# Performance work log

Measured on AMD Instinct MI355X. Metric: run time of the kernel, lower is better.

## Reference

```python
import jax, jax.numpy as jnp
import numpy as np

N = 50000
E = 800000
G = 2500  # number of graphs


def setup_inputs() -> dict:
    key = jax.random.key(0)
    ks = jax.random.split(key, 10)
    x = jax.random.normal(ks[0], (N, 128), dtype=jnp.float32)
    edge_index = jax.random.randint(ks[1], (2, E), 0, N, dtype=jnp.int64)
    batch = jnp.sort(jax.random.randint(ks[2], (N,), 0, G, dtype=jnp.int64))
    def lin(k, fan_in, shape):
        return jax.random.normal(k, shape, dtype=jnp.float32) / np.sqrt(fan_in)
    return {
        'x': x, 'edge_index': edge_index, 'batch': batch,
        'W1': lin(ks[3], 128, (128, 64)), 'b1': jnp.zeros((64,), jnp.float32),
        'W2': lin(ks[4], 64, (64, 64)),  'b2': jnp.zeros((64,), jnp.float32),
        'W3': lin(ks[5], 64, (64, 64)),  'b3': jnp.zeros((64,), jnp.float32),
        'Wp1': lin(ks[6], 64, (64, 64)), 'bp1': jnp.zeros((64,), jnp.float32),
        'Wp2': lin(ks[7], 64, (64, 32)), 'bp2': jnp.zeros((32,), jnp.float32),
    }


def _gcn_norm(edge_index, n_nodes):
    # PyG GCNConv default: add self-loops, symmetric normalization
    loops = jnp.arange(n_nodes, dtype=edge_index.dtype)
    src = jnp.concatenate([edge_index[0], loops])
    dst = jnp.concatenate([edge_index[1], loops])
    deg = jax.ops.segment_sum(jnp.ones_like(dst, dtype=jnp.float32), dst,
                              num_segments=n_nodes)
    dis = jnp.where(deg > 0, jax.lax.rsqrt(deg), 0.0)
    norm = dis[src] * dis[dst]  # [E + N]
    return src, dst, norm


def _gcn_conv(x, W, b, src, dst, norm, n_nodes):
    h = x @ W                                   # transform first (small dim)
    m = h[src] * norm[:, None]                  # gather + scale
    out = jax.ops.segment_sum(m, dst, num_segments=n_nodes)  # scatter-add
    return out + b


def reference(x, edge_index, batch, W1, b1, W2, b2, W3, b3, Wp1, bp1, Wp2, bp2):
    n_nodes = x.shape[0]
    src, dst, norm = _gcn_norm(edge_index, n_nodes)
    x1 = jax.nn.relu(_gcn_conv(x, W1, b1, src, dst, norm, n_nodes))
    x2 = jax.nn.relu(_gcn_conv(x1, W2, b2, src, dst, norm, n_nodes))
    x3 = jax.nn.relu(_gcn_conv(x2, W3, b3, src, dst, norm, n_nodes))
    h = x1 + x2 + x3
    # global_mean_pool
    sums = jax.ops.segment_sum(h, batch, num_segments=G)
    counts = jax.ops.segment_sum(jnp.ones((n_nodes,), jnp.float32), batch,
                                 num_segments=G)
    pooled = sums / jnp.maximum(counts, 1.0)[:, None]
    z = jax.nn.relu(pooled @ Wp1 + bp1) @ Wp2 + bp2
    return z
```

## Files before the change

kernel.cpp:

```cpp
#include <hip/hip_runtime.h>
#include <math.h>


typedef short short8 __attribute__((ext_vector_type(8)));
typedef float f32x4 __attribute__((ext_vector_type(4)));

__device__ inline float bf2f(unsigned short h) {
    return __uint_as_float((unsigned)h << 16);
}
__device__ inline unsigned short f2bf(float f) {
    unsigned u = __float_as_uint(f);
    return (unsigned short)((u + (0x7FFFu + ((u >> 16) & 1u))) >> 16);
}
__device__ inline void bh8f(short8 u, float4& a, float4& b) {
    a.x = bf2f((unsigned short)u[0]); a.y = bf2f((unsigned short)u[1]);
    a.z = bf2f((unsigned short)u[2]); a.w = bf2f((unsigned short)u[3]);
    b.x = bf2f((unsigned short)u[4]); b.y = bf2f((unsigned short)u[5]);
    b.z = bf2f((unsigned short)u[6]); b.w = bf2f((unsigned short)u[7]);
}
__device__ inline float4 f4fma(float s, float4 a, float4 acc) {
    acc.x += s * a.x; acc.y += s * a.y; acc.z += s * a.z; acc.w += s * a.w;
    return acc;
}

__global__ void kA_hist(const int* __restrict__ dst, int* __restrict__ hist,
                        int E, int chunk) {
    __shared__ int h[256];
    int t = threadIdx.x;
    h[t] = 0;
    __syncthreads();
    int e0 = blockIdx.x * chunk;
    int e1 = min(e0 + chunk, E);
    for (int e = e0 + t; e < e1; e += 256) atomicAdd(&h[dst[e] >> 8], 1);
    __syncthreads();
    hist[blockIdx.x * 256 + t] = h[t];
}

__global__ void kA_colscan(const int* __restrict__ hist, int* __restrict__ cursorA,
                           int* __restrict__ tot) {
    __shared__ int s[256];
    int t = threadIdx.x;
    int k = blockIdx.x;
    int v = hist[t * 256 + k];
    s[t] = v;
    __syncthreads();
    for (int st = 1; st < 256; st <<= 1) {
        int u = s[t];
        if (t >= st) u += s[t - st];
        __syncthreads();
        s[t] = u;
        __syncthreads();
    }
    cursorA[t * 256 + k] = s[t] - v;
    if (t == 255) tot[k] = s[255];
}

__global__ void kA_scatter(const int* __restrict__ src, const int* __restrict__ dst,
                           const int* __restrict__ cursorA, const int* __restrict__ tot,
                           unsigned* __restrict__ ebuf, int E, int chunk) {
    __shared__ int s[256];
    __shared__ int cur[256];
    int t = threadIdx.x;
    s[t] = tot[t];
    __syncthreads();
    for (int st = 1; st < 256; st <<= 1) {
        int u = s[t];
        if (t >= st) u += s[t - st];
        __syncthreads();
        s[t] = u;
        __syncthreads();
    }
    int bstart = (t == 0) ? 0 : s[t - 1];
    cur[t] = cursorA[blockIdx.x * 256 + t] + bstart;
    __syncthreads();
    int e0 = blockIdx.x * chunk;
    int e1 = min(e0 + chunk, E);
    for (int e = e0 + t; e < e1; e += 256) {
        int d = dst[e];
        int p = atomicAdd(&cur[d >> 8], 1);
        ebuf[p] = ((unsigned)(d & 255) << 24) | (unsigned)src[e];
    }
}

__global__ void kB1(const unsigned* __restrict__ ebuf, const int* __restrict__ tot,
                    float* __restrict__ dis, int* __restrict__ offs, int N, int E) {
    __shared__ int s[256];
    __shared__ int h[256];
    int t = threadIdx.x;
    int k = blockIdx.x;
    s[t] = tot[t];
    __syncthreads();
    for (int st = 1; st < 256; st <<= 1) {
        int u = s[t];
        if (t >= st) u += s[t - st];
        __syncthreads();
        s[t] = u;
        __syncthreads();
    }
    int lo = (k == 0) ? 0 : s[k - 1];
    int hi = s[k];
    h[t] = 0;
    __syncthreads();
    for (int p = lo + t; p < hi; p += 256) atomicAdd(&h[ebuf[p] >> 24], 1);
    __syncthreads();
    int c = h[t];
    int node = k * 256 + t;
    if (node < N) dis[node] = rsqrtf((float)(c + 1));
    s[t] = c;
    __syncthreads();
    for (int st = 1; st < 256; st <<= 1) {
        int u = s[t];
        if (t >= st) u += s[t - st];
        __syncthreads();
        s[t] = u;
        __syncthreads();
    }
    if (node < N) offs[node] = lo + s[t] - c;
    if (node == N - 1) offs[N] = E;
}

__global__ void kB2(const unsigned* __restrict__ ebuf, const int* __restrict__ tot,
                    const float* __restrict__ dis, const int* __restrict__ offs,
                    float2* __restrict__ col2, int N, int E) {
    __shared__ int s[256];
    __shared__ int cur[256];
    int t = threadIdx.x;
    int k = blockIdx.x;
    s[t] = tot[t];
    __syncthreads();
    for (int st = 1; st < 256; st <<= 1) {
        int u = s[t];
        if (t >= st) u += s[t - st];
        __syncthreads();
        s[t] = u;
        __syncthreads();
    }
    int lo = (k == 0) ? 0 : s[k - 1];
    int hi = s[k];
    int node = k * 256 + t;
    cur[t] = (node < N) ? offs[node] : 0;
    __syncthreads();
    for (int p = lo + t; p < hi; p += 256) {
        unsigned e = ebuf[p];
        int srcI = (int)(e & 0x00FFFFFFu);
        int q = atomicAdd(&cur[e >> 24], 1);
        col2[q] = make_float2(__int_as_float(srcI), dis[srcI]);
    }
}


template <int K>
__global__ __launch_bounds__(256) void k_gemm_f32(const float* __restrict__ X,
                                                  const float* __restrict__ W,
                                                  unsigned short* __restrict__ H, int n) {
    __shared__ short wt[64 * K];
    int t = threadIdx.x;
    for (int idx = t; idx < 64 * K; idx += 256) {
        int k = idx >> 6, ch = idx & 63;
        wt[ch * K + k] = (short)f2bf(W[idx]);
    }
    __syncthreads();
    int wave = t >> 6, lane = t & 63;
    int q = lane >> 4, l = lane & 15;
    int tile = blockIdx.x * 4 + wave;
    if (tile * 16 >= n) return;
    int node = tile * 16 + l;
    short8 afr[4][K / 32];
#pragma unroll
    for (int mb = 0; mb < 4; mb++)
#pragma unroll
        for (int s = 0; s < K / 32; s++)
            afr[mb][s] = *(const short8*)(wt + (mb * 16 + l) * K + s * 32 + q * 8);
    f32x4 acc[4] = {};
    const float* xr = X + (size_t)node * K + q * 8;
#pragma unroll
    for (int s = 0; s < K / 32; s++) {
        float4 xa = *(const float4*)(xr + s * 32);
        float4 xb = *(const float4*)(xr + s * 32 + 4);
        short8 bfr;
        bfr[0] = (short)f2bf(xa.x); bfr[1] = (short)f2bf(xa.y);
        bfr[2] = (short)f2bf(xa.z); bfr[3] = (short)f2bf(xa.w);
        bfr[4] = (short)f2bf(xb.x); bfr[5] = (short)f2bf(xb.y);
        bfr[6] = (short)f2bf(xb.z); bfr[7] = (short)f2bf(xb.w);
#pragma unroll
        for (int mb = 0; mb < 4; mb++)
            acc[mb] = __builtin_amdgcn_mfma_f32_16x16x32_bf16(afr[mb][s], bfr, acc[mb], 0, 0, 0);
    }
#pragma unroll
    for (int mb = 0; mb < 4; mb++) {
        ushort4 u;
        u.x = f2bf(acc[mb][0]); u.y = f2bf(acc[mb][1]);
        u.z = f2bf(acc[mb][2]); u.w = f2bf(acc[mb][3]);
        ushort4* slab = (ushort4*)H + (size_t)(mb >> 1) * (size_t)n * 8;
        slab[(size_t)node * 8 + (mb & 1) * 4 + q] = u;
    }
}

__global__ __launch_bounds__(256) void k_gemm_bf(const unsigned short* __restrict__ Xb,
                                                 const float* __restrict__ W,
                                                 unsigned short* __restrict__ H, int n) {
    const int K = 64;
    __shared__ short wt[64 * K];
    int t = threadIdx.x;
    for (int idx = t; idx < 64 * K; idx += 256) {
        int k = idx >> 6, ch = idx & 63;
        wt[ch * K + k] = (short)f2bf(W[idx]);
    }
    __syncthreads();
    int wave = t >> 6, lane = t & 63;
    int q = lane >> 4, l = lane & 15;
    int tile = blockIdx.x * 4 + wave;
    if (tile * 16 >= n) return;
    int node = tile * 16 + l;
    short8 afr[4][2];
#pragma unroll
    for (int mb = 0; mb < 4; mb++)
#pragma unroll
        for (int s = 0; s < 2; s++)
            afr[mb][s] = *(const short8*)(wt + (mb * 16 + l) * K + s * 32 + q * 8);
    f32x4 acc[4] = {};
    const short8* xr = (const short8*)(Xb + (size_t)node * 64);
#pragma unroll
    for (int s = 0; s < 2; s++) {
        short8 bfr = xr[s * 4 + q];
#pragma unroll
        for (int mb = 0; mb < 4; mb++)
            acc[mb] = __builtin_amdgcn_mfma_f32_16x16x32_bf16(afr[mb][s], bfr, acc[mb], 0, 0, 0);
    }
#pragma unroll
    for (int mb = 0; mb < 4; mb++) {
        ushort4 u;
        u.x = f2bf(acc[mb][0]); u.y = f2bf(acc[mb][1]);
        u.z = f2bf(acc[mb][2]); u.w = f2bf(acc[mb][3]);
        ushort4* slab = (ushort4*)H + (size_t)(mb >> 1) * (size_t)n * 8;
        slab[(size_t)node * 8 + (mb & 1) * 4 + q] = u;
    }
}

__global__ void k_agg(const unsigned short* __restrict__ H, const float2* __restrict__ col2,
                      const int* __restrict__ offs, const float* __restrict__ dis,
                      const float* __restrict__ bias,
                      const unsigned short* __restrict__ add1,
                      const unsigned short* __restrict__ add2,
                      unsigned short* __restrict__ OutB, float* __restrict__ OutS,
                      int n, int tiles) {
    int B = blockIdx.x;
    int xx = B & 7;
    int h = xx >> 2;
    int within = (B >> 3) * 4 + (xx & 3);
    if (within >= tiles) return;
    int t = threadIdx.x;
    int node = within * 64 + (t >> 2);
    if (node >= n) return;
    int lane = t & 3;
    const short8* Hs = (const short8*)(H + (size_t)h * (size_t)n * 32);
    float dn = dis[node];
    float4 acc0, acc1;
    bh8f(Hs[(size_t)node * 4 + lane], acc0, acc1);
    acc0.x *= dn; acc0.y *= dn; acc0.z *= dn; acc0.w *= dn;
    acc1.x *= dn; acc1.y *= dn; acc1.z *= dn; acc1.w *= dn;
    int lo = offs[node], hi = offs[node + 1];
    int p = lo;
    for (; p + 4 <= hi; p += 4) {
        float2 e0 = col2[p], e1 = col2[p + 1], e2 = col2[p + 2], e3 = col2[p + 3];
        short8 g0 = Hs[(size_t)__float_as_int(e0.x) * 4 + lane];
        short8 g1 = Hs[(size_t)__float_as_int(e1.x) * 4 + lane];
        short8 g2 = Hs[(size_t)__float_as_int(e2.x) * 4 + lane];
        short8 g3 = Hs[(size_t)__float_as_int(e3.x) * 4 + lane];
        float4 a, b;
        bh8f(g0, a, b); acc0 = f4fma(e0.y, a, acc0); acc1 = f4fma(e0.y, b, acc1);
        bh8f(g1, a, b); acc0 = f4fma(e1.y, a, acc0); acc1 = f4fma(e1.y, b, acc1);
        bh8f(g2, a, b); acc0 = f4fma(e2.y, a, acc0); acc1 = f4fma(e2.y, b, acc1);
        bh8f(g3, a, b); acc0 = f4fma(e3.y, a, acc0); acc1 = f4fma(e3.y, b, acc1);
    }
    for (; p < hi; p++) {
        float2 e = col2[p];
        float4 a, b;
        bh8f(Hs[(size_t)__float_as_int(e.x) * 4 + lane], a, b);
        acc0 = f4fma(e.y, a, acc0);
        acc1 = f4fma(e.y, b, acc1);
    }
    const float4* bias4 = (const float4*)bias;
    float4 bb0 = bias4[h * 8 + lane * 2];
    float4 bb1 = bias4[h * 8 + lane * 2 + 1];
    float4 v0, v1;
    v0.x = fmaxf(acc0.x * dn + bb0.x, 0.f);
    v0.y = fmaxf(acc0.y * dn + bb0.y, 0.f);
    v0.z = fmaxf(acc0.z * dn + bb0.z, 0.f);
    v0.w = fmaxf(acc0.w * dn + bb0.w, 0.f);
    v1.x = fmaxf(acc1.x * dn + bb1.x, 0.f);
    v1.y = fmaxf(acc1.y * dn + bb1.y, 0.f);
    v1.z = fmaxf(acc1.z * dn + bb1.z, 0.f);
    v1.w = fmaxf(acc1.w * dn + bb1.w, 0.f);
    size_t slot = (size_t)node * 8 + h * 4 + lane;
    if (OutS) {
        float4 a10, a11, a20, a21;
        bh8f(((const short8*)add1)[slot], a10, a11);
        bh8f(((const short8*)add2)[slot], a20, a21);
        v0.x += a10.x + a20.x; v0.y += a10.y + a20.y;
        v0.z += a10.z + a20.z; v0.w += a10.w + a20.w;
        v1.x += a11.x + a21.x; v1.y += a11.y + a21.y;
        v1.z += a11.z + a21.z; v1.w += a11.w + a21.w;
        float4* S4 = (float4*)OutS;
        size_t oi = (size_t)node * 16 + (size_t)(h * 4 + lane) * 2;
        S4[oi] = v0;
        S4[oi + 1] = v1;
    } else {
        short8 o;
        o[0] = (short)f2bf(v0.x); o[1] = (short)f2bf(v0.y);
        o[2] = (short)f2bf(v0.z); o[3] = (short)f2bf(v0.w);
        o[4] = (short)f2bf(v1.x); o[5] = (short)f2bf(v1.y);
        o[6] = (short)f2bf(v1.z); o[7] = (short)f2bf(v1.w);
        ((short8*)OutB)[slot] = o;
    }
}

__global__ void k_poolhead(const float* __restrict__ S, const int* __restrict__ batch,
                           const float* __restrict__ Wp1, const float* __restrict__ bp1,
                           const float* __restrict__ Wp2, const float* __restrict__ bp2,
                           float* __restrict__ out, int n, int G) {
    int g = blockIdx.x;
    int j = threadIdx.x;
    int a = 0, b = n;
    while (a < b) { int m = (a + b) >> 1; if (batch[m] < g) a = m + 1; else b = m; }
    int beg = a;
    b = n;
    while (a < b) { int m = (a + b) >> 1; if (batch[m] < g + 1) a = m + 1; else b = m; }
    int end = a;
    float sum = 0.f;
    int i = beg;
    for (; i + 2 <= end; i += 2)
        sum += S[(size_t)i * 64 + j] + S[(size_t)(i + 1) * 64 + j];
    if (i < end) sum += S[(size_t)i * 64 + j];
    float cnt = (float)(end - beg);
    float p = sum / fmaxf(cnt, 1.f);
    __shared__ float ps[64];
    __shared__ float ts[64];
    ps[j] = p;
    __syncthreads();
    float t1 = bp1[j];
#pragma unroll 8
    for (int k = 0; k < 64; k++) t1 += ps[k] * Wp1[k * 64 + j];
    t1 = fmaxf(t1, 0.f);
    ts[j] = t1;
    __syncthreads();
    if (j < 32) {
        float o = bp2[j];
#pragma unroll 8
        for (int k = 0; k < 64; k++) o += ts[k] * Wp2[k * 32 + j];
        out[(size_t)g * 32 + j] = o;
    }
}

extern "C" void kernel_launch(void* const* d_in, const int* in_sizes, int n_in,
                              void* d_out, int out_size, void* d_ws, size_t ws_size,
                              hipStream_t stream) {
    const float* x   = (const float*)d_in[0];
    const int*   ei  = (const int*)d_in[1];
    const int*   bat = (const int*)d_in[2];
    const float* W1  = (const float*)d_in[3];
    const float* b1  = (const float*)d_in[4];
    const float* W2  = (const float*)d_in[5];
    const float* b2  = (const float*)d_in[6];
    const float* W3  = (const float*)d_in[7];
    const float* b3  = (const float*)d_in[8];
    const float* Wp1 = (const float*)d_in[9];
    const float* bp1 = (const float*)d_in[10];
    const float* Wp2 = (const float*)d_in[11];
    const float* bp2 = (const float*)d_in[12];

    int N = in_sizes[0] / 128;
    int E = in_sizes[1] / 2;
    int G = out_size / 32;
    const int* src = ei;
    const int* dst = ei + E;

    char* w = (char*)d_ws;
    auto alloc = [&](size_t bytes) -> void* {
        void* p = (void*)w;
        w += (bytes + 255) & ~(size_t)255;
        return p;
    };
    int NB = (N + 255) / 256;
    int*            offs    = (int*)alloc((size_t)(N + 1) * 4);
    float2*         col2    = (float2*)alloc((size_t)E * 8);
    float*          dis     = (float*)alloc((size_t)N * 4);
    int*            hist    = (int*)alloc((size_t)256 * 256 * 4);
    int*            cursorA = (int*)alloc((size_t)256 * 256 * 4);
    int*            tot     = (int*)alloc((size_t)256 * 4);
    unsigned*       ebuf    = (unsigned*)alloc((size_t)E * 4);
    unsigned short* Hb      = (unsigned short*)alloc((size_t)N * 64 * 2);
    unsigned short* X1      = (unsigned short*)alloc((size_t)N * 64 * 2);
    unsigned short* X2      = (unsigned short*)alloc((size_t)N * 64 * 2);
    float*          S       = (float*)alloc((size_t)N * 64 * 4);

    int chunk = (E + 255) / 256;

    kA_hist<<<256, 256, 0, stream>>>(dst, hist, E, chunk);
    kA_colscan<<<256, 256, 0, stream>>>(hist, cursorA, tot);
    kA_scatter<<<256, 256, 0, stream>>>(src, dst, cursorA, tot, ebuf, E, chunk);
    kB1<<<NB, 256, 0, stream>>>(ebuf, tot, dis, offs, N, E);
    kB2<<<NB, 256, 0, stream>>>(ebuf, tot, dis, offs, col2, N, E);

    int ggemm = ((N >> 4) + 3) / 4;
    int tiles = (N + 63) / 64;
    int gagg  = ((tiles + 3) / 4) * 8;
    k_gemm_f32<128><<<ggemm, 256, 0, stream>>>(x, W1, Hb, N);
    k_agg<<<gagg, 256, 0, stream>>>(Hb, col2, offs, dis, b1, nullptr, nullptr, X1, nullptr, N, tiles);
    k_gemm_bf<<<ggemm, 256, 0, stream>>>(X1, W2, Hb, N);
    k_agg<<<gagg, 256, 0, stream>>>(Hb, col2, offs, dis, b2, nullptr, nullptr, X2, nullptr, N, tiles);
    k_gemm_bf<<<ggemm, 256, 0, stream>>>(X2, W3, Hb, N);
    k_agg<<<gagg, 256, 0, stream>>>(Hb, col2, offs, dis, b3, X1, X2, nullptr, S, N, tiles);

    k_poolhead<<<G, 64, 0, stream>>>(S, bat, Wp1, bp1, Wp2, bp2, (float*)d_out, N, G);
}
```

Before: 245.0 us.

## Pack CSR edges into 32 bits and aggregate full 64-channel rows per pass

Each CSR edge entry becomes one 32-bit word holding a 16-bit source index and an fp16 copy of the source's inverse-sqrt degree, replacing the 8-byte float2. The transformed features H are stored as contiguous 64-channel bf16 rows instead of two 32-channel slabs. Aggregation now uses 8 lanes per node and covers all channels in one pass, instead of two half-channel passes that each re-read the edge list. This cuts edge-list traffic and gives full-row gathers. The 16-bit index only holds while N < 65536, and the fp16 weight adds a little rounding.

```diff
diff --git a/kernel.cpp b/kernel.cpp
--- a/kernel.cpp
+++ b/kernel.cpp
@@ -11,6 +11,16 @@
 __device__ inline unsigned short f2bf(float f) {
     unsigned u = __float_as_uint(f);
     return (unsigned short)((u + (0x7FFFu + ((u >> 16) & 1u))) >> 16);
+}
+__device__ inline unsigned short f2h(float f) {
+    union { _Float16 h; unsigned short u; } c;
+    c.h = (_Float16)f;
+    return c.u;
+}
+__device__ inline float h2f(unsigned short u) {
+    union { unsigned short u; _Float16 h; } c;
+    c.u = u;
+    return (float)c.h;
 }
 __device__ inline void bh8f(short8 u, float4& a, float4& b) {
     a.x = bf2f((unsigned short)u[0]); a.y = bf2f((unsigned short)u[1]);
@@ -121,7 +131,7 @@
 
 __global__ void kB2(const unsigned* __restrict__ ebuf, const int* __restrict__ tot,
                     const float* __restrict__ dis, const int* __restrict__ offs,
-                    float2* __restrict__ col2, int N, int E) {
+                    unsigned* __restrict__ col, int N, int E) {
     __shared__ int s[256];
     __shared__ int cur[256];
     int t = threadIdx.x;
@@ -144,7 +154,7 @@
         unsigned e = ebuf[p];
         int srcI = (int)(e & 0x00FFFFFFu);
         int q = atomicAdd(&cur[e >> 24], 1);
-        col2[q] = make_float2(__int_as_float(srcI), dis[srcI]);
+        col[q] = ((unsigned)f2h(dis[srcI]) << 16) | (unsigned)srcI;
     }
 }
 
@@ -191,8 +201,7 @@
         ushort4 u;
         u.x = f2bf(acc[mb][0]); u.y = f2bf(acc[mb][1]);
         u.z = f2bf(acc[mb][2]); u.w = f2bf(acc[mb][3]);
-        ushort4* slab = (ushort4*)H + (size_t)(mb >> 1) * (size_t)n * 8;
-        slab[(size_t)node * 8 + (mb & 1) * 4 + q] = u;
+        ((ushort4*)H)[(size_t)node * 16 + mb * 4 + q] = u;
     }
 }
 
@@ -232,57 +241,55 @@
         ushort4 u;
         u.x = f2bf(acc[mb][0]); u.y = f2bf(acc[mb][1]);
         u.z = f2bf(acc[mb][2]); u.w = f2bf(acc[mb][3]);
-        ushort4* slab = (ushort4*)H + (size_t)(mb >> 1) * (size_t)n * 8;
-        slab[(size_t)node * 8 + (mb & 1) * 4 + q] = u;
-    }
-}
-
-__global__ void k_agg(const unsigned short* __restrict__ H, const float2* __restrict__ col2,
+        ((ushort4*)H)[(size_t)node * 16 + mb * 4 + q] = u;
+    }
+}
+
+__global__ void k_agg(const unsigned short* __restrict__ H, const unsigned* __restrict__ col,
                       const int* __restrict__ offs, const float* __restrict__ dis,
                       const float* __restrict__ bias,
                       const unsigned short* __restrict__ add1,
                       const unsigned short* __restrict__ add2,
-                      unsigned short* __restrict__ OutB, float* __restrict__ OutS,
-                      int n, int tiles) {
-    int B = blockIdx.x;
-    int xx = B & 7;
-    int h = xx >> 2;
-    int within = (B >> 3) * 4 + (xx & 3);
-    if (within >= tiles) return;
-    int t = threadIdx.x;
-    int node = within * 64 + (t >> 2);
+                      unsigned short* __restrict__ OutB, float* __restrict__ OutS, int n) {
+    int t = threadIdx.x;
+    int node = blockIdx.x * 32 + (t >> 3);
     if (node >= n) return;
-    int lane = t & 3;
-    const short8* Hs = (const short8*)(H + (size_t)h * (size_t)n * 32);
+    int lane = t & 7;
+    const short8* Hs = (const short8*)H;
     float dn = dis[node];
     float4 acc0, acc1;
-    bh8f(Hs[(size_t)node * 4 + lane], acc0, acc1);
+    bh8f(Hs[(size_t)node * 8 + lane], acc0, acc1);
     acc0.x *= dn; acc0.y *= dn; acc0.z *= dn; acc0.w *= dn;
     acc1.x *= dn; acc1.y *= dn; acc1.z *= dn; acc1.w *= dn;
     int lo = offs[node], hi = offs[node + 1];
     int p = lo;
     for (; p + 4 <= hi; p += 4) {
-        float2 e0 = col2[p], e1 = col2[p + 1], e2 = col2[p + 2], e3 = col2[p + 3];
-        short8 g0 = Hs[(size_t)__float_as_int(e0.x) * 4 + lane];
-        short8 g1 = Hs[(size_t)__float_as_int(e1.x) * 4 + lane];
-        short8 g2 = Hs[(size_t)__float_as_int(e2.x) * 4 + lane];
-        short8 g3 = Hs[(size_t)__float_as_int(e3.x) * 4 + lane];
+        unsigned e0 = col[p], e1 = col[p + 1], e2 = col[p + 2], e3 = col[p + 3];
+        short8 g0 = Hs[(size_t)(e0 & 0xFFFFu) * 8 + lane];
+        short8 g1 = Hs[(size_t)(e1 & 0xFFFFu) * 8 + lane];
+        short8 g2 = Hs[(size_t)(e2 & 0xFFFFu) * 8 + lane];
+        short8 g3 = Hs[(size_t)(e3 & 0xFFFFu) * 8 + lane];
+        float w0 = h2f((unsigned short)(e0 >> 16));
+        float w1 = h2f((unsigned short)(e1 >> 16));
+        float w2 = h2f((unsigned short)(e2 >> 16));
+        float w3 = h2f((unsigned short)(e3 >> 16));
         float4 a, b;
-        bh8f(g0, a, b); acc0 = f4fma(e0.y, a, acc0); acc1 = f4fma(e0.y, b, acc1);
-        bh8f(g1, a, b); acc0 = f4fma(e1.y, a, acc0); acc1 = f4fma(e1.y, b, acc1);
-        bh8f(g2, a, b); acc0 = f4fma(e2.y, a, acc0); acc1 = f4fma(e2.y, b, acc1);
-        bh8f(g3, a, b); acc0 = f4fma(e3.y, a, acc0); acc1 = f4fma(e3.y, b, acc1);
+        bh8f(g0, a, b); acc0 = f4fma(w0, a, acc0); acc1 = f4fma(w0, b, acc1);
+        bh8f(g1, a, b); acc0 = f4fma(w1, a, acc0); acc1 = f4fma(w1, b, acc1);
+        bh8f(g2, a, b); acc0 = f4fma(w2, a, acc0); acc1 = f4fma(w2, b, acc1);
+        bh8f(g3, a, b); acc0 = f4fma(w3, a, acc0); acc1 = f4fma(w3, b, acc1);
     }
     for (; p < hi; p++) {
-        float2 e = col2[p];
+        unsigned e = col[p];
+        float w = h2f((unsigned short)(e >> 16));
         float4 a, b;
-        bh8f(Hs[(size_t)__float_as_int(e.x) * 4 + lane], a, b);
-        acc0 = f4fma(e.y, a, acc0);
-        acc1 = f4fma(e.y, b, acc1);
+        bh8f(Hs[(size_t)(e & 0xFFFFu) * 8 + lane], a, b);
+        acc0 = f4fma(w, a, acc0);
+        acc1 = f4fma(w, b, acc1);
     }
     const float4* bias4 = (const float4*)bias;
-    float4 bb0 = bias4[h * 8 + lane * 2];
-    float4 bb1 = bias4[h * 8 + lane * 2 + 1];
+    float4 bb0 = bias4[lane * 2];
+    float4 bb1 = bias4[lane * 2 + 1];
     float4 v0, v1;
     v0.x = fmaxf(acc0.x * dn + bb0.x, 0.f);
     v0.y = fmaxf(acc0.y * dn + bb0.y, 0.f);
@@ -292,7 +299,7 @@
     v1.y = fmaxf(acc1.y * dn + bb1.y, 0.f);
     v1.z = fmaxf(acc1.z * dn + bb1.z, 0.f);
     v1.w = fmaxf(acc1.w * dn + bb1.w, 0.f);
-    size_t slot = (size_t)node * 8 + h * 4 + lane;
+    size_t slot = (size_t)node * 8 + lane;
     if (OutS) {
         float4 a10, a11, a20, a21;
         bh8f(((const short8*)add1)[slot], a10, a11);
@@ -302,7 +309,7 @@
         v1.x += a11.x + a21.x; v1.y += a11.y + a21.y;
         v1.z += a11.z + a21.z; v1.w += a11.w + a21.w;
         float4* S4 = (float4*)OutS;
-        size_t oi = (size_t)node * 16 + (size_t)(h * 4 + lane) * 2;
+        size_t oi = (size_t)node * 16 + (size_t)lane * 2;
         S4[oi] = v0;
         S4[oi + 1] = v1;
     } else {
@@ -383,7 +390,7 @@
     };
     int NB = (N + 255) / 256;
     int*            offs    = (int*)alloc((size_t)(N + 1) * 4);
-    float2*         col2    = (float2*)alloc((size_t)E * 8);
+    unsigned*       col     = (unsigned*)alloc((size_t)E * 4);
     float*          dis     = (float*)alloc((size_t)N * 4);
     int*            hist    = (int*)alloc((size_t)256 * 256 * 4);
     int*            cursorA = (int*)alloc((size_t)256 * 256 * 4);
@@ -400,17 +407,16 @@
     kA_colscan<<<256, 256, 0, stream>>>(hist, cursorA, tot);
     kA_scatter<<<256, 256, 0, stream>>>(src, dst, cursorA, tot, ebuf, E, chunk);
     kB1<<<NB, 256, 0, stream>>>(ebuf, tot, dis, offs, N, E);
-    kB2<<<NB, 256, 0, stream>>>(ebuf, tot, dis, offs, col2, N, E);
+    kB2<<<NB, 256, 0, stream>>>(ebuf, tot, dis, offs, col, N, E);
 
     int ggemm = ((N >> 4) + 3) / 4;
-    int tiles = (N + 63) / 64;
-    int gagg  = ((tiles + 3) / 4) * 8;
+    int gagg  = (N + 31) / 32;
     k_gemm_f32<128><<<ggemm, 256, 0, stream>>>(x, W1, Hb, N);
-    k_agg<<<gagg, 256, 0, stream>>>(Hb, col2, offs, dis, b1, nullptr, nullptr, X1, nullptr, N, tiles);
+    k_agg<<<gagg, 256, 0, stream>>>(Hb, col, offs, dis, b1, nullptr, nullptr, X1, nullptr, N);
     k_gemm_bf<<<ggemm, 256, 0, stream>>>(X1, W2, Hb, N);
-    k_agg<<<gagg, 256, 0, stream>>>(Hb, col2, offs, dis, b2, nullptr, nullptr, X2, nullptr, N, tiles);
+    k_agg<<<gagg, 256, 0, stream>>>(Hb, col, offs, dis, b2, nullptr, nullptr, X2, nullptr, N);
     k_gemm_bf<<<ggemm, 256, 0, stream>>>(X2, W3, Hb, N);
-    k_agg<<<gagg, 256, 0, stream>>>(Hb, col2, offs, dis, b3, X1, X2, nullptr, S, N, tiles);
+    k_agg<<<gagg, 256, 0, stream>>>(Hb, col, offs, dis, b3, X1, X2, nullptr, S, N);
 
     k_poolhead<<<G, 64, 0, stream>>>(S, bat, Wp1, bp1, Wp2, bp2, (float*)d_out, N, G);
 }
```

Result: faster. 237.0 us (-3.3%).
